# Kernel tuning notes

Hardware: AMD Instinct MI355X
Metric: run time of the kernel (lower is better)

Reference implementation:

```python
import jax, jax.numpy as jnp
import numpy as np

# Dims matching init_kwargs / input_specs
H = 8          # num_heads
S = 256        # seq_len_src
T = 1024       # seq_len_tgt
D = 64         # head_dim
SZ_B = 16      # batch size
B = SZ_B * H   # flattened batch*heads = 128
RATIO = T // S # subsampling_ratio = 4
NEG = -100.0   # pad value used by the skewing trick


def setup_inputs() -> dict:
    key = jax.random.key(0)
    kq, k1, k2 = jax.random.split(key, 3)
    q = jax.random.normal(kq, (B, T, D), dtype=jnp.float32)
    e1 = jax.random.normal(k1, (H * S, D), dtype=jnp.float32)
    e2 = jax.random.normal(k2, (H * S, D), dtype=jnp.float32)
    return {"q": q, "e1": e1, "e2": e2}


def _rel_scores(q, e):
    # torch: e.repeat(sz_b,1,1).view(sz_b*H, S, D); einsum('bld,bmd->blm', q, e)
    # equivalent: per-head einsum without materializing the tiled e
    qh = q.reshape(SZ_B, H, T, D)
    eh = e.reshape(H, S, D)
    return jnp.einsum('bhtd,hsd->bhts', qh, eh).reshape(B, T, S)


def _skew(r, prepend_pad):
    # Music-Transformer skewing: (B,T,S) -> reinterpret as (B,S,T), pad a
    # -100 column (front for e1 path, back for e2 path), pad -100 rows to
    # (B,T,T+1), then reshape by S to shift scores into relative positions.
    r = r.reshape(B, S, T)
    pad_col = jnp.full((B, S, 1), NEG, dtype=r.dtype)
    parts = [pad_col, r] if prepend_pad else [r, pad_col]
    r = jnp.concatenate(parts, axis=2)                       # (B, S, T+1)
    if T > S:
        pad_rows = jnp.full((B, T - S, T + 1), NEG, dtype=r.dtype)
        r = jnp.concatenate([r, pad_rows], axis=1)           # (B, T, T+1)
    r = r.reshape(B, -1, S)                                  # (B, T*(T+1)//S, S)
    if prepend_pad:
        r = r[:, 1:]
    return r[:, :T]                                          # (B, T, S)


def reference(q, e1, e2):
    r1 = _skew(_rel_scores(q, e1), prepend_pad=True)
    r2 = _skew(_rel_scores(q, e2), prepend_pad=False)
    # masks_up: triu(k=1); masks_down: triu(k=0).flip(0).flip(1) == tril(k=0)
    # both repeat_interleave'd by RATIO along the row (tgt) axis -> (T, S)
    up = jnp.repeat(jnp.triu(jnp.ones((S, S), dtype=bool), 1), RATIO, axis=0)
    down = jnp.repeat(jnp.tril(jnp.ones((S, S), dtype=bool), 0), RATIO, axis=0)
    r1 = jnp.where(up[None, :, :], jnp.array(0.0, r1.dtype), r1)
    r2 = jnp.where(down[None, :, :], jnp.array(0.0, r2.dtype), r2)
    return r1 + r2
```

## Files before the change

### kernel.cpp

```cpp
#include <hip/hip_runtime.h>
#include <hip/hip_bf16.h>

#define NH   8
#define NS   256
#define NT   1024
#define ND   64
#define NB   128

typedef __attribute__((ext_vector_type(4))) float f32x4;
typedef __attribute__((ext_vector_type(8))) short short8;

__device__ __forceinline__ short f2bf(float f) {
    union { float f; unsigned u; } v; v.f = f;
    unsigned r = v.u + 0x7FFFu + ((v.u >> 16) & 1u);
    return (short)(r >> 16);
}

__global__ __launch_bounds__(256) void srel_kernel(
    const float* __restrict__ q, const float* __restrict__ e1,
    const float* __restrict__ e2, float* __restrict__ out)
{
    const int h   = blockIdx.x >> 8;
    const int a   = blockIdx.x & 255;
    const int tid = threadIdx.x;

    __shared__ __align__(16) unsigned short lA[64 * 72];
    __shared__ __align__(16) unsigned short lB[NS * 72];

    {
        const int m    = tid >> 2;
        const int part = tid & 3;
        const int b    = (m >> 2) * NH + h;
        const int t    = a * 4 + (m & 3);
        const float4* src = (const float4*)(q + ((size_t)b * NT + t) * ND + part * 16);
        unsigned short* dst = lA + m * 72 + part * 16;
        float4 v0 = src[0], v1 = src[1], v2 = src[2], v3 = src[3];
        short8 p0, p1;
        p0[0]=f2bf(v0.x); p0[1]=f2bf(v0.y); p0[2]=f2bf(v0.z); p0[3]=f2bf(v0.w);
        p0[4]=f2bf(v1.x); p0[5]=f2bf(v1.y); p0[6]=f2bf(v1.z); p0[7]=f2bf(v1.w);
        p1[0]=f2bf(v2.x); p1[1]=f2bf(v2.y); p1[2]=f2bf(v2.z); p1[3]=f2bf(v2.w);
        p1[4]=f2bf(v3.x); p1[5]=f2bf(v3.y); p1[6]=f2bf(v3.z); p1[7]=f2bf(v3.w);
        *(short8*)dst       = p0;
        *(short8*)(dst + 8) = p1;
    }

    #pragma unroll
    for (int p = 0; p < 4; ++p) {
        const int s    = p * 64 + (tid >> 2);
        const int part = tid & 3;
        const float* base = (s <= a)
            ? (e1 + ((size_t)(h * NS + (255 - a + s))) * ND)
            : (e2 + ((size_t)(h * NS + (s - a)))       * ND);
        const float4* src = (const float4*)(base + part * 16);
        unsigned short* dst = lB + s * 72 + part * 16;
        float4 v0 = src[0], v1 = src[1], v2 = src[2], v3 = src[3];
        short8 p0, p1;
        p0[0]=f2bf(v0.x); p0[1]=f2bf(v0.y); p0[2]=f2bf(v0.z); p0[3]=f2bf(v0.w);
        p0[4]=f2bf(v1.x); p0[5]=f2bf(v1.y); p0[6]=f2bf(v1.z); p0[7]=f2bf(v1.w);
        p1[0]=f2bf(v2.x); p1[1]=f2bf(v2.y); p1[2]=f2bf(v2.z); p1[3]=f2bf(v2.w);
        p1[4]=f2bf(v3.x); p1[5]=f2bf(v3.y); p1[6]=f2bf(v3.z); p1[7]=f2bf(v3.w);
        *(short8*)dst       = p0;
        *(short8*)(dst + 8) = p1;
    }

    __syncthreads();

    const int wave = tid >> 6;
    const int lane = tid & 63;
    const int lrow = lane & 15;
    const int quad = lane >> 4;

    f32x4 acc[4][4] = {};
    #pragma unroll
    for (int kk = 0; kk < 64; kk += 32) {
        short8 afr[4], bfr[4];
        #pragma unroll
        for (int tm = 0; tm < 4; ++tm)
            afr[tm] = *(const short8*)(lA + (tm * 16 + lrow) * 72 + kk + quad * 8);
        #pragma unroll
        for (int tn = 0; tn < 4; ++tn)
            bfr[tn] = *(const short8*)(lB + (wave * 64 + tn * 16 + lrow) * 72 + kk + quad * 8);
        #pragma unroll
        for (int tm = 0; tm < 4; ++tm)
            #pragma unroll
            for (int tn = 0; tn < 4; ++tn)
                acc[tm][tn] = __builtin_amdgcn_mfma_f32_16x16x32_bf16(
                    afr[tm], bfr[tn], acc[tm][tn], 0, 0, 0);
    }

    #pragma unroll
    for (int tm = 0; tm < 4; ++tm) {
        #pragma unroll
        for (int r = 0; r < 4; ++r) {
            const int m = tm * 16 + quad * 4 + r;
            const int b = (m >> 2) * NH + h;
            const int t = a * 4 + (m & 3);
            float* orow = out + ((size_t)b * NT + t) * NS + wave * 64 + lrow;
            #pragma unroll
            for (int tn = 0; tn < 4; ++tn)
                orow[tn * 16] = acc[tm][tn][r];
        }
    }
}

extern "C" void kernel_launch(void* const* d_in, const int* in_sizes, int n_in,
                              void* d_out, int out_size, void* d_ws, size_t ws_size,
                              hipStream_t stream) {
    (void)in_sizes; (void)n_in; (void)d_ws; (void)ws_size; (void)out_size;
    const float* q  = (const float*)d_in[0];
    const float* e1 = (const float*)d_in[1];
    const float* e2 = (const float*)d_in[2];
    float* out = (float*)d_out;
    srel_kernel<<<dim3(NH * NS), dim3(256), 0, stream>>>(q, e1, e2, out);
}
```

Measured before the change: 169.6 us.

## Pre-convert e to bf16, DMA into swizzled LDS, coalesce output stores via LDS

Adds a small prologue kernel that converts e1 and e2 to bf16 once into workspace, so each block loads the gathered relative-position rows with direct global-to-LDS loads instead of fp32 loads plus per-element conversion. LDS tiles now use an XOR swizzle in place of padding, and the accumulator is staged through LDS in two halves so each output row is written with coalesced 16-byte vector stores. The cost is an extra kernel launch, a workspace buffer, and added barriers in the epilogue.

```diff
diff --git a/kernel.cpp b/kernel.cpp
--- a/kernel.cpp
+++ b/kernel.cpp
@@ -6,6 +6,7 @@
 #define NT   1024
 #define ND   64
 #define NB   128
+#define ESZ  (NH * NS * ND)
 
 typedef __attribute__((ext_vector_type(4))) float f32x4;
 typedef __attribute__((ext_vector_type(8))) short short8;
@@ -16,16 +17,53 @@
     return (short)(r >> 16);
 }
 
-__global__ __launch_bounds__(256) void srel_kernel(
-    const float* __restrict__ q, const float* __restrict__ e1,
-    const float* __restrict__ e2, float* __restrict__ out)
+__global__ __launch_bounds__(256) void cvt_e_kernel(
+    const float* __restrict__ e1, const float* __restrict__ e2,
+    unsigned short* __restrict__ eb)
+{
+    const int i = (blockIdx.x * 256 + threadIdx.x) * 8;
+    const float* src = (i < ESZ) ? (e1 + i) : (e2 + (i - ESZ));
+    float4 v0 = ((const float4*)src)[0];
+    float4 v1 = ((const float4*)src)[1];
+    short8 p;
+    p[0]=f2bf(v0.x); p[1]=f2bf(v0.y); p[2]=f2bf(v0.z); p[3]=f2bf(v0.w);
+    p[4]=f2bf(v1.x); p[5]=f2bf(v1.y); p[6]=f2bf(v1.z); p[7]=f2bf(v1.w);
+    *(short8*)(eb + i) = p;
+}
+
+__global__ __launch_bounds__(256, 4) void srel_kernel(
+    const float* __restrict__ q, const unsigned short* __restrict__ eb,
+    float* __restrict__ out)
 {
     const int h   = blockIdx.x >> 8;
     const int a   = blockIdx.x & 255;
     const int tid = threadIdx.x;
+    const int wave = tid >> 6;
+    const int lane = tid & 63;
 
-    __shared__ __align__(16) unsigned short lA[64 * 72];
-    __shared__ __align__(16) unsigned short lB[NS * 72];
+    __shared__ __align__(16) char smem[64*64*2 + NS*64*2];
+    unsigned short* lA = (unsigned short*)smem;
+    unsigned short* lB = (unsigned short*)(smem + 64*64*2);
+    float* fbuf = (float*)smem;
+
+    {
+        const unsigned short* eb1 = eb;
+        const unsigned short* eb2 = eb + ESZ;
+        const int srow = lane >> 3;
+        const int physc = lane & 7;
+        #pragma unroll
+        for (int rnd = 0; rnd < 8; ++rnd) {
+            const int s = rnd * 32 + wave * 8 + srow;
+            const int j = physc ^ (s & 7);
+            const unsigned short* src = (s <= a)
+                ? (eb1 + (h * NS + 255 - a + s) * ND + j * 8)
+                : (eb2 + (h * NS + s - a)       * ND + j * 8);
+            __builtin_amdgcn_global_load_lds(
+                (const __attribute__((address_space(1))) void*)src,
+                (__attribute__((address_space(3))) void*)(lB + (rnd * 32 + wave * 8) * 64),
+                16, 0, 0);
+        }
+    }
 
     {
         const int m    = tid >> 2;
@@ -33,53 +71,32 @@
         const int b    = (m >> 2) * NH + h;
         const int t    = a * 4 + (m & 3);
         const float4* src = (const float4*)(q + ((size_t)b * NT + t) * ND + part * 16);
-        unsigned short* dst = lA + m * 72 + part * 16;
         float4 v0 = src[0], v1 = src[1], v2 = src[2], v3 = src[3];
         short8 p0, p1;
         p0[0]=f2bf(v0.x); p0[1]=f2bf(v0.y); p0[2]=f2bf(v0.z); p0[3]=f2bf(v0.w);
         p0[4]=f2bf(v1.x); p0[5]=f2bf(v1.y); p0[6]=f2bf(v1.z); p0[7]=f2bf(v1.w);
         p1[0]=f2bf(v2.x); p1[1]=f2bf(v2.y); p1[2]=f2bf(v2.z); p1[3]=f2bf(v2.w);
         p1[4]=f2bf(v3.x); p1[5]=f2bf(v3.y); p1[6]=f2bf(v3.z); p1[7]=f2bf(v3.w);
-        *(short8*)dst       = p0;
-        *(short8*)(dst + 8) = p1;
-    }
-
-    #pragma unroll
-    for (int p = 0; p < 4; ++p) {
-        const int s    = p * 64 + (tid >> 2);
-        const int part = tid & 3;
-        const float* base = (s <= a)
-            ? (e1 + ((size_t)(h * NS + (255 - a + s))) * ND)
-            : (e2 + ((size_t)(h * NS + (s - a)))       * ND);
-        const float4* src = (const float4*)(base + part * 16);
-        unsigned short* dst = lB + s * 72 + part * 16;
-        float4 v0 = src[0], v1 = src[1], v2 = src[2], v3 = src[3];
-        short8 p0, p1;
-        p0[0]=f2bf(v0.x); p0[1]=f2bf(v0.y); p0[2]=f2bf(v0.z); p0[3]=f2bf(v0.w);
-        p0[4]=f2bf(v1.x); p0[5]=f2bf(v1.y); p0[6]=f2bf(v1.z); p0[7]=f2bf(v1.w);
-        p1[0]=f2bf(v2.x); p1[1]=f2bf(v2.y); p1[2]=f2bf(v2.z); p1[3]=f2bf(v2.w);
-        p1[4]=f2bf(v3.x); p1[5]=f2bf(v3.y); p1[6]=f2bf(v3.z); p1[7]=f2bf(v3.w);
-        *(short8*)dst       = p0;
-        *(short8*)(dst + 8) = p1;
+        const int sw = m & 7;
+        *(short8*)(lA + m * 64 + (((2*part)   ^ sw) * 8)) = p0;
+        *(short8*)(lA + m * 64 + (((2*part+1) ^ sw) * 8)) = p1;
     }
 
     __syncthreads();
 
-    const int wave = tid >> 6;
-    const int lane = tid & 63;
     const int lrow = lane & 15;
     const int quad = lane >> 4;
-
     f32x4 acc[4][4] = {};
     #pragma unroll
-    for (int kk = 0; kk < 64; kk += 32) {
+    for (int kk2 = 0; kk2 < 2; ++kk2) {
+        const int swz = ((4 * kk2 + quad) ^ (lrow & 7)) * 8;
         short8 afr[4], bfr[4];
         #pragma unroll
         for (int tm = 0; tm < 4; ++tm)
-            afr[tm] = *(const short8*)(lA + (tm * 16 + lrow) * 72 + kk + quad * 8);
+            afr[tm] = *(const short8*)(lA + (tm * 16 + lrow) * 64 + swz);
         #pragma unroll
         for (int tn = 0; tn < 4; ++tn)
-            bfr[tn] = *(const short8*)(lB + (wave * 64 + tn * 16 + lrow) * 72 + kk + quad * 8);
+            bfr[tn] = *(const short8*)(lB + (wave * 64 + tn * 16 + lrow) * 64 + swz);
         #pragma unroll
         for (int tm = 0; tm < 4; ++tm)
             #pragma unroll
@@ -89,16 +106,28 @@
     }
 
     #pragma unroll
-    for (int tm = 0; tm < 4; ++tm) {
+    for (int c = 0; c < 2; ++c) {
+        __syncthreads();
         #pragma unroll
-        for (int r = 0; r < 4; ++r) {
-            const int m = tm * 16 + quad * 4 + r;
-            const int b = (m >> 2) * NH + h;
-            const int t = a * 4 + (m & 3);
-            float* orow = out + ((size_t)b * NT + t) * NS + wave * 64 + lrow;
+        for (int tmh = 0; tmh < 2; ++tmh) {
+            const int tm = c * 2 + tmh;
             #pragma unroll
-            for (int tn = 0; tn < 4; ++tn)
-                orow[tn * 16] = acc[tm][tn][r];
+            for (int r = 0; r < 4; ++r) {
+                const int rl = tmh * 16 + quad * 4 + r;
+                #pragma unroll
+                for (int tn = 0; tn < 4; ++tn)
+                    fbuf[rl * 260 + wave * 64 + tn * 16 + lrow] = acc[tm][tn][r];
+            }
+        }
+        __syncthreads();
+        #pragma unroll
+        for (int i = 0; i < 8; ++i) {
+            const int rl = i * 4 + wave;
+            const int m  = c * 32 + rl;
+            const int b  = (m >> 2) * NH + h;
+            const int t  = a * 4 + (m & 3);
+            f32x4 v = *(const f32x4*)(fbuf + rl * 260 + lane * 4);
+            *(f32x4*)(out + ((size_t)b * NT + t) * NS + lane * 4) = v;
         }
     }
 }
@@ -106,10 +135,13 @@
 extern "C" void kernel_launch(void* const* d_in, const int* in_sizes, int n_in,
                               void* d_out, int out_size, void* d_ws, size_t ws_size,
                               hipStream_t stream) {
-    (void)in_sizes; (void)n_in; (void)d_ws; (void)ws_size; (void)out_size;
+    (void)in_sizes; (void)n_in; (void)ws_size; (void)out_size;
     const float* q  = (const float*)d_in[0];
     const float* e1 = (const float*)d_in[1];
     const float* e2 = (const float*)d_in[2];
     float* out = (float*)d_out;
-    srel_kernel<<<dim3(NH * NS), dim3(256), 0, stream>>>(q, e1, e2, out);
+    unsigned short* eb = (unsigned short*)d_ws;
+
+    cvt_e_kernel<<<dim3(2 * ESZ / (256 * 8)), dim3(256), 0, stream>>>(e1, e2, eb);
+    srel_kernel<<<dim3(NH * NS), dim3(256), 0, stream>>>(q, eb, out);
 }
```

Measured after the change: 166.6 us. No clear change (-1.8%).

## Stage output tile in LDS for coalesced nontemporal stores; swizzle LDS operands

Applied to the files above, without the earlier changes.

The accumulator tile is written into a shared-memory float buffer and then read back row-wise, so each wave stores whole 1 KB output rows as 16-byte nontemporal vector stores. Before, lanes wrote scattered scalar floats. The bf16 operand tiles drop row padding in favour of an XOR swizzle, q loads become nontemporal, and a launch_bounds occupancy hint is added. The shared buffer grows to about 66 KB and there are two extra barriers, which may limit how many blocks fit per CU. The odd 258-float row stride can also misalign the 16-byte LDS reads.

```diff
diff --git a/kernel.cpp b/kernel.cpp
--- a/kernel.cpp
+++ b/kernel.cpp
@@ -5,7 +5,6 @@
 #define NS   256
 #define NT   1024
 #define ND   64
-#define NB   128
 
 typedef __attribute__((ext_vector_type(4))) float f32x4;
 typedef __attribute__((ext_vector_type(8))) short short8;
@@ -16,32 +15,39 @@
     return (short)(r >> 16);
 }
 
-__global__ __launch_bounds__(256) void srel_kernel(
+__global__ __launch_bounds__(256, 4) void srel_kernel(
     const float* __restrict__ q, const float* __restrict__ e1,
     const float* __restrict__ e2, float* __restrict__ out)
 {
-    const int h   = blockIdx.x >> 8;
-    const int a   = blockIdx.x & 255;
-    const int tid = threadIdx.x;
+    const int h    = blockIdx.x >> 8;
+    const int a    = blockIdx.x & 255;
+    const int tid  = threadIdx.x;
+    const int wave = tid >> 6;
+    const int lane = tid & 63;
 
-    __shared__ __align__(16) unsigned short lA[64 * 72];
-    __shared__ __align__(16) unsigned short lB[NS * 72];
+    __shared__ __align__(16) char smem[64 * 258 * 4];
+    unsigned short* lA = (unsigned short*)smem;
+    unsigned short* lB = (unsigned short*)(smem + 64*64*2);
+    float* fbuf = (float*)smem;
 
     {
         const int m    = tid >> 2;
         const int part = tid & 3;
         const int b    = (m >> 2) * NH + h;
         const int t    = a * 4 + (m & 3);
-        const float4* src = (const float4*)(q + ((size_t)b * NT + t) * ND + part * 16);
-        unsigned short* dst = lA + m * 72 + part * 16;
-        float4 v0 = src[0], v1 = src[1], v2 = src[2], v3 = src[3];
+        const f32x4* src = (const f32x4*)(q + ((size_t)b * NT + t) * ND + part * 16);
+        f32x4 v0 = __builtin_nontemporal_load(src);
+        f32x4 v1 = __builtin_nontemporal_load(src + 1);
+        f32x4 v2 = __builtin_nontemporal_load(src + 2);
+        f32x4 v3 = __builtin_nontemporal_load(src + 3);
         short8 p0, p1;
-        p0[0]=f2bf(v0.x); p0[1]=f2bf(v0.y); p0[2]=f2bf(v0.z); p0[3]=f2bf(v0.w);
-        p0[4]=f2bf(v1.x); p0[5]=f2bf(v1.y); p0[6]=f2bf(v1.z); p0[7]=f2bf(v1.w);
-        p1[0]=f2bf(v2.x); p1[1]=f2bf(v2.y); p1[2]=f2bf(v2.z); p1[3]=f2bf(v2.w);
-        p1[4]=f2bf(v3.x); p1[5]=f2bf(v3.y); p1[6]=f2bf(v3.z); p1[7]=f2bf(v3.w);
-        *(short8*)dst       = p0;
-        *(short8*)(dst + 8) = p1;
+        p0[0]=f2bf(v0[0]); p0[1]=f2bf(v0[1]); p0[2]=f2bf(v0[2]); p0[3]=f2bf(v0[3]);
+        p0[4]=f2bf(v1[0]); p0[5]=f2bf(v1[1]); p0[6]=f2bf(v1[2]); p0[7]=f2bf(v1[3]);
+        p1[0]=f2bf(v2[0]); p1[1]=f2bf(v2[1]); p1[2]=f2bf(v2[2]); p1[3]=f2bf(v2[3]);
+        p1[4]=f2bf(v3[0]); p1[5]=f2bf(v3[1]); p1[6]=f2bf(v3[2]); p1[7]=f2bf(v3[3]);
+        const int sw = m & 7;
+        *(short8*)(lA + m * 64 + (((2*part)   ^ sw) * 8)) = p0;
+        *(short8*)(lA + m * 64 + (((2*part+1) ^ sw) * 8)) = p1;
     }
 
     #pragma unroll
@@ -49,37 +55,35 @@
         const int s    = p * 64 + (tid >> 2);
         const int part = tid & 3;
         const float* base = (s <= a)
-            ? (e1 + ((size_t)(h * NS + (255 - a + s))) * ND)
-            : (e2 + ((size_t)(h * NS + (s - a)))       * ND);
-        const float4* src = (const float4*)(base + part * 16);
-        unsigned short* dst = lB + s * 72 + part * 16;
-        float4 v0 = src[0], v1 = src[1], v2 = src[2], v3 = src[3];
+            ? (e1 + (size_t)(h * NS + (255 - a + s)) * ND)
+            : (e2 + (size_t)(h * NS + (s - a))       * ND);
+        const f32x4* src = (const f32x4*)(base + part * 16);
+        f32x4 v0 = src[0], v1 = src[1], v2 = src[2], v3 = src[3];
         short8 p0, p1;
-        p0[0]=f2bf(v0.x); p0[1]=f2bf(v0.y); p0[2]=f2bf(v0.z); p0[3]=f2bf(v0.w);
-        p0[4]=f2bf(v1.x); p0[5]=f2bf(v1.y); p0[6]=f2bf(v1.z); p0[7]=f2bf(v1.w);
-        p1[0]=f2bf(v2.x); p1[1]=f2bf(v2.y); p1[2]=f2bf(v2.z); p1[3]=f2bf(v2.w);
-        p1[4]=f2bf(v3.x); p1[5]=f2bf(v3.y); p1[6]=f2bf(v3.z); p1[7]=f2bf(v3.w);
-        *(short8*)dst       = p0;
-        *(short8*)(dst + 8) = p1;
+        p0[0]=f2bf(v0[0]); p0[1]=f2bf(v0[1]); p0[2]=f2bf(v0[2]); p0[3]=f2bf(v0[3]);
+        p0[4]=f2bf(v1[0]); p0[5]=f2bf(v1[1]); p0[6]=f2bf(v1[2]); p0[7]=f2bf(v1[3]);
+        p1[0]=f2bf(v2[0]); p1[1]=f2bf(v2[1]); p1[2]=f2bf(v2[2]); p1[3]=f2bf(v2[3]);
+        p1[4]=f2bf(v3[0]); p1[5]=f2bf(v3[1]); p1[6]=f2bf(v3[2]); p1[7]=f2bf(v3[3]);
+        const int sw = s & 7;
+        *(short8*)(lB + s * 64 + (((2*part)   ^ sw) * 8)) = p0;
+        *(short8*)(lB + s * 64 + (((2*part+1) ^ sw) * 8)) = p1;
     }
 
     __syncthreads();
 
-    const int wave = tid >> 6;
-    const int lane = tid & 63;
     const int lrow = lane & 15;
     const int quad = lane >> 4;
-
     f32x4 acc[4][4] = {};
     #pragma unroll
-    for (int kk = 0; kk < 64; kk += 32) {
+    for (int kk2 = 0; kk2 < 2; ++kk2) {
+        const int swz = ((4 * kk2 + quad) ^ (lrow & 7)) * 8;
         short8 afr[4], bfr[4];
         #pragma unroll
         for (int tm = 0; tm < 4; ++tm)
-            afr[tm] = *(const short8*)(lA + (tm * 16 + lrow) * 72 + kk + quad * 8);
+            afr[tm] = *(const short8*)(lA + (tm * 16 + lrow) * 64 + swz);
         #pragma unroll
         for (int tn = 0; tn < 4; ++tn)
-            bfr[tn] = *(const short8*)(lB + (wave * 64 + tn * 16 + lrow) * 72 + kk + quad * 8);
+            bfr[tn] = *(const short8*)(lB + (wave * 64 + tn * 16 + lrow) * 64 + swz);
         #pragma unroll
         for (int tm = 0; tm < 4; ++tm)
             #pragma unroll
@@ -88,18 +92,24 @@
                     afr[tm], bfr[tn], acc[tm][tn], 0, 0, 0);
     }
 
+    __syncthreads();
     #pragma unroll
-    for (int tm = 0; tm < 4; ++tm) {
+    for (int tm = 0; tm < 4; ++tm)
         #pragma unroll
         for (int r = 0; r < 4; ++r) {
-            const int m = tm * 16 + quad * 4 + r;
-            const int b = (m >> 2) * NH + h;
-            const int t = a * 4 + (m & 3);
-            float* orow = out + ((size_t)b * NT + t) * NS + wave * 64 + lrow;
+            const int rl = tm * 16 + quad * 4 + r;
             #pragma unroll
             for (int tn = 0; tn < 4; ++tn)
-                orow[tn * 16] = acc[tm][tn][r];
+                fbuf[rl * 258 + wave * 64 + tn * 16 + lrow] = acc[tm][tn][r];
         }
+    __syncthreads();
+    #pragma unroll
+    for (int i = 0; i < 16; ++i) {
+        const int m = i * 4 + wave;
+        const int b = (m >> 2) * NH + h;
+        const int t = a * 4 + (m & 3);
+        f32x4 v = *(const f32x4*)(fbuf + m * 258 + lane * 4);
+        __builtin_nontemporal_store(v, (f32x4*)(out + ((size_t)b * NT + t) * NS + lane * 4));
     }
 }
 
```

Measured after the change: 180.6 us. +6.5%, slower.
